# Optimization experiments

Measured on AMD Instinct MI355X. Metric: run time of the kernel, lower is better.

The kernel has to match this reference:

```python
import jax, jax.numpy as jnp
import numpy as np

B, N, D, H = 2, 2048, 1024, 16
HD = D // H
SCALE = HD ** -0.5


def setup_inputs() -> dict:
    key = jax.random.key(0)
    ks = jax.random.split(key, 5)
    s = D ** -0.5  # keep activations well-scaled like torch Linear init
    return {
        "x": jax.random.normal(ks[0], (B, N, D), jnp.float32),
        "Wq": jax.random.normal(ks[1], (D, D), jnp.float32) * s,
        "bq": jnp.zeros((D,), jnp.float32),
        "Wk": jax.random.normal(ks[2], (D, D), jnp.float32) * s,
        "bk": jnp.zeros((D,), jnp.float32),
        "Wv": jax.random.normal(ks[3], (D, D), jnp.float32) * s,
        "bv": jnp.zeros((D,), jnp.float32),
        "Wo": jax.random.normal(ks[4], (D, D), jnp.float32) * s,
        "bo": jnp.zeros((D,), jnp.float32),
    }


def reference(x, Wq, bq, Wk, bk, Wv, bv, Wo, bo):
    # projections: [B,N,D] -> [B,H,N,HD]
    def split_heads(t):
        return t.reshape(B, N, H, HD).transpose(0, 2, 1, 3)

    q = split_heads(x @ Wq + bq)
    k = split_heads(x @ Wk + bk)
    v = split_heads(x @ Wv + bv)
    # eager attention: explicit [B,H,N,N] scores, matching the torch module
    attn = jnp.einsum("bhnd,bhmd->bhnm", q, k) * SCALE
    attn = jax.nn.softmax(attn, axis=-1)
    out = jnp.einsum("bhnm,bhmd->bhnd", attn, v)
    out = out.transpose(0, 2, 1, 3).reshape(B, N, D)
    return out @ Wo + bo
```

## Files before the change

kernel.cpp:

```cpp
#include <hip/hip_runtime.h>
#include <hip/hip_bf16.h>

typedef __attribute__((ext_vector_type(8))) short bf16x8;
typedef __attribute__((ext_vector_type(4))) float f32x4;
typedef __attribute__((ext_vector_type(4))) unsigned short us4;
typedef __attribute__((ext_vector_type(8))) unsigned short us8;
typedef unsigned short u16;

#define NB 2
#define NSEQ 2048
#define DM 1024
#define NH 16
#define HD 64
#define NTOK (NB*NSEQ)
#define QK_SCALE (0.125f * 1.4426950408889634f)

__device__ __forceinline__ u16 f2b(float f) {
  __hip_bfloat16 h = __float2bfloat16(f);
  return __builtin_bit_cast(u16, h);
}

__device__ __forceinline__ unsigned cvtpk(float a, float b) {
  unsigned r;
  asm("v_cvt_pk_bf16_f32 %0, %1, %2" : "=v"(r) : "v"(a), "v"(b));
  return r;
}

__device__ __forceinline__ void gload16(const void* g, void* l) {
  __builtin_amdgcn_global_load_lds((__attribute__((address_space(1))) void*)g,
                                   (__attribute__((address_space(3))) void*)l, 16, 0, 0);
}

__global__ __launch_bounds__(256) void k_convx(const float* __restrict__ x, u16* __restrict__ xb) {
  const int idx = (blockIdx.x * 256 + threadIdx.x) * 8;
  const float4 v0 = *(const float4*)(x + idx);
  const float4 v1 = *(const float4*)(x + idx + 4);
  us8 o;
  o[0]=f2b(v0.x); o[1]=f2b(v0.y); o[2]=f2b(v0.z); o[3]=f2b(v0.w);
  o[4]=f2b(v1.x); o[5]=f2b(v1.y); o[6]=f2b(v1.z); o[7]=f2b(v1.w);
  *(us8*)(xb + idx) = o;
}

__global__ __launch_bounds__(256) void k_twt4(const float* __restrict__ W0, const float* __restrict__ W1,
                                              const float* __restrict__ W2, const float* __restrict__ W3,
                                              u16* __restrict__ T0, u16* __restrict__ T1,
                                              u16* __restrict__ T2, u16* __restrict__ T3) {
  const float* W = (blockIdx.z == 0) ? W0 : (blockIdx.z == 1) ? W1 : (blockIdx.z == 2) ? W2 : W3;
  u16* WT = (blockIdx.z == 0) ? T0 : (blockIdx.z == 1) ? T1 : (blockIdx.z == 2) ? T2 : T3;
  __shared__ float tile[64][68];
  const int n0 = blockIdx.x * 64, k0 = blockIdx.y * 64;
  const int tr = threadIdx.x >> 4, tc = (threadIdx.x & 15) * 4;
#pragma unroll
  for (int rr = 0; rr < 4; ++rr) {
    const int r = rr * 16 + tr;
    *(float4*)&tile[r][tc] = *(const float4*)&W[(size_t)(k0 + r) * DM + n0 + tc];
  }
  __syncthreads();
#pragma unroll
  for (int rr = 0; rr < 4; ++rr) {
    const int nr = rr * 16 + tr;
    us4 o;
#pragma unroll
    for (int e = 0; e < 4; ++e) o[e] = f2b(tile[tc + e][nr]);
    *(us4*)&WT[(size_t)(n0 + nr) * DM + k0 + tc] = o;
  }
}

__global__ __launch_bounds__(256) void k_gemm_qkv(
    const u16* __restrict__ xb,
    const u16* __restrict__ WqT, const u16* __restrict__ WkT, const u16* __restrict__ WvT,
    const float* __restrict__ bq, const float* __restrict__ bk, const float* __restrict__ bv,
    u16* __restrict__ Qb, u16* __restrict__ Kb, u16* __restrict__ Vtb)
{
  const int z = blockIdx.z;
  const bool isV = (z == 2);
  const u16* Ap = (z == 0) ? WqT : (z == 1) ? WkT : xb;
  const u16* Bt = isV ? WvT : xb;
  const float* bp = (z == 0) ? bq : (z == 1) ? bk : bv;
  const float scale = (z == 0) ? QK_SCALE : 1.0f;
  u16* outp = (z == 0) ? Qb : (z == 1) ? Kb : Vtb;
  const int i0 = isV ? blockIdx.x * 128 : blockIdx.y * 128;
  const int j0 = isV ? blockIdx.y * 128 : blockIdx.x * 128;

  __shared__ char smem[32 * 1024];
  const int tid = threadIdx.x, lane = tid & 63, wv = tid >> 6;
  const int li = lane & 15, g = lane >> 4;
  const int wi = wv >> 1, wj = wv & 1;

  f32x4 acc[4][4];
#pragma unroll
  for (int a = 0; a < 4; ++a)
#pragma unroll
    for (int b = 0; b < 4; ++b) acc[a][b] = f32x4{0.f, 0.f, 0.f, 0.f};

  auto stage = [&](int kt, int buf) {
#pragma unroll
    for (int c = 0; c < 2; ++c) {
      const int lg = c * 256 + tid;
      const int r = lg >> 2, ch = (lg & 3) ^ (r & 3);
      gload16(Ap + (size_t)(i0 + r) * 1024 + kt * 32 + ch * 8,
              smem + buf * 16384 + lg * 16);
      gload16(Bt + (size_t)(j0 + r) * 1024 + kt * 32 + ch * 8,
              smem + buf * 16384 + 8192 + lg * 16);
    }
  };

  stage(0, 0);

  for (int kt = 0; kt < 32; ++kt) {
    __syncthreads();
    if (kt + 1 < 32) stage(kt + 1, (kt + 1) & 1);
    const char* As = smem + (kt & 1) * 16384;
    const char* Bs = As + 8192;
    bf16x8 af[4], bfr[4];
#pragma unroll
    for (int it = 0; it < 4; ++it) {
      const int ri = 64 * wi + 16 * it + li;
      af[it] = *(const bf16x8*)(As + ri * 64 + ((g * 16) ^ ((ri & 3) << 4)));
      const int rj = 64 * wj + 16 * it + li;
      bfr[it] = *(const bf16x8*)(Bs + rj * 64 + ((g * 16) ^ ((rj & 3) << 4)));
    }
#pragma unroll
    for (int it = 0; it < 4; ++it)
#pragma unroll
      for (int jt = 0; jt < 4; ++jt)
        acc[it][jt] = __builtin_amdgcn_mfma_f32_16x16x32_bf16(af[it], bfr[jt], acc[it][jt], 0, 0, 0);
  }

#pragma unroll
  for (int it = 0; it < 4; ++it) {
    const int ib = i0 + 64 * wi + 16 * it + 4 * g;
    f32x4 b4;
    if (!isV) b4 = *(const f32x4*)(bp + ib);
#pragma unroll
    for (int jt = 0; jt < 4; ++jt) {
      const int j = j0 + 64 * wj + 16 * jt + li;
      f32x4 v = acc[it][jt];
      if (!isV) {
        v += b4;
        v *= scale;
        us4 pk; pk[0]=f2b(v[0]); pk[1]=f2b(v[1]); pk[2]=f2b(v[2]); pk[3]=f2b(v[3]);
        *(us4*)(outp + (size_t)j * 1024 + ib) = pk;
      } else {
        const float bj = bp[j];
        v[0] += bj; v[1] += bj; v[2] += bj; v[3] += bj;
        us4 pk; pk[0]=f2b(v[0]); pk[1]=f2b(v[1]); pk[2]=f2b(v[2]); pk[3]=f2b(v[3]);
        const size_t addr = ((size_t)(ib >> 11) * 1024 + j) * 2048 + (ib & 2047);
        *(us4*)(outp + addr) = pk;
      }
    }
  }
}

__global__ __launch_bounds__(256) void k_gemm_out(
    const u16* __restrict__ A, const u16* __restrict__ Bt, const float* __restrict__ bias,
    float* __restrict__ outp)
{
  __shared__ char smem[48 * 1024];
  const int tid = threadIdx.x, lane = tid & 63, wv = tid >> 6;
  const int li = lane & 15, g = lane >> 4;
  const int i0 = blockIdx.y * 128, j0 = blockIdx.x * 64;

  f32x4 acc[2][4];
#pragma unroll
  for (int a = 0; a < 2; ++a)
#pragma unroll
    for (int b = 0; b < 4; ++b) acc[a][b] = f32x4{0.f, 0.f, 0.f, 0.f};

  auto stage = [&](int kt, int buf) {
#pragma unroll
    for (int c = 0; c < 4; ++c) {
      const int lg = c * 256 + tid;
      const int r = lg >> 3, ch = (lg & 7) ^ (r & 7);
      gload16(A + (size_t)(i0 + r) * 1024 + kt * 64 + ch * 8,
              smem + buf * 24576 + lg * 16);
    }
#pragma unroll
    for (int c = 0; c < 2; ++c) {
      const int lg = c * 256 + tid;
      const int r = lg >> 3, ch = (lg & 7) ^ (r & 7);
      gload16(Bt + (size_t)(j0 + r) * 1024 + kt * 64 + ch * 8,
              smem + buf * 24576 + 16384 + lg * 16);
    }
  };

  stage(0, 0);

  for (int kt = 0; kt < 16; ++kt) {
    __syncthreads();
    if (kt + 1 < 16) stage(kt + 1, (kt + 1) & 1);
    const char* As = smem + (kt & 1) * 24576;
    const char* Bs = As + 16384;
#pragma unroll
    for (int ks = 0; ks < 2; ++ks) {
      bf16x8 af[2], bfr[4];
#pragma unroll
      for (int it = 0; it < 2; ++it) {
        const int ri = 32 * wv + 16 * it + li;
        af[it] = *(const bf16x8*)(As + ri * 128 + ((ks * 64 + g * 16) ^ ((ri & 7) << 4)));
      }
#pragma unroll
      for (int jt = 0; jt < 4; ++jt) {
        const int rj = 16 * jt + li;
        bfr[jt] = *(const bf16x8*)(Bs + rj * 128 + ((ks * 64 + g * 16) ^ ((rj & 7) << 4)));
      }
#pragma unroll
      for (int it = 0; it < 2; ++it)
#pragma unroll
        for (int jt = 0; jt < 4; ++jt)
          acc[it][jt] = __builtin_amdgcn_mfma_f32_16x16x32_bf16(af[it], bfr[jt], acc[it][jt], 0, 0, 0);
    }
  }

#pragma unroll
  for (int it = 0; it < 2; ++it) {
    const int ib = i0 + 32 * wv + 16 * it + 4 * g;
    const f32x4 b4 = *(const f32x4*)(bias + ib);
#pragma unroll
    for (int jt = 0; jt < 4; ++jt) {
      const int j = j0 + 16 * jt + li;
      f32x4 v = acc[it][jt] + b4;
      *(f32x4*)(outp + (size_t)j * 1024 + ib) = v;
    }
  }
}

__global__ __launch_bounds__(256, 2) void k_attn(const u16* __restrict__ Q, const u16* __restrict__ K,
                                                 const u16* __restrict__ Vt, u16* __restrict__ O)
{
  __shared__ char smem[48 * 1024];
  const int tid = threadIdx.x, lane = tid & 63, w = tid >> 6;
  const int li = lane & 15, g = lane >> 4;

  const int vid = blockIdx.x;
  const int u = vid >> 3;
  const int bh = (vid & 7) * 4 + (u >> 4);
  const int qt = u & 15;
  const int b = bh >> 4, h = bh & 15;
  const int n0 = qt * 128;
  const size_t tokbase = (size_t)b * NSEQ;
  const int iq = 16 * w + li;

  bf16x8 qf[2][2];
#pragma unroll
  for (int grp = 0; grp < 2; ++grp)
#pragma unroll
    for (int ks = 0; ks < 2; ++ks)
      qf[grp][ks] = *(const bf16x8*)(Q + (tokbase + n0 + 64 * grp + iq) * 1024 + h * 64 + 32 * ks + 8 * g);

  bf16x8 ones;
#pragma unroll
  for (int e = 0; e < 8; ++e) ones[e] = (short)0x3F80;

  f32x4 oacc[2][4];
#pragma unroll
  for (int grp = 0; grp < 2; ++grp)
#pragma unroll
    for (int dt = 0; dt < 4; ++dt) oacc[grp][dt] = f32x4{0.f, 0.f, 0.f, 0.f};
  f32x4 ls[2] = {f32x4{0.f,0.f,0.f,0.f}, f32x4{0.f,0.f,0.f,0.f}};

  const u16* Kb = K + tokbase * 1024 + h * 64;
  const u16* Vb = Vt + (size_t)bh * 64 * 2048;

  auto stage = [&](int t, int buf) {
    const int jn = t * 64;
#pragma unroll
    for (int c = 0; c < 2; ++c) {
      const int lg = c * 256 + tid;
      const int r = lg >> 3, ch = (lg & 7) ^ (r & 7);
      gload16(Kb + (size_t)(jn + r) * 1024 + ch * 8, smem + buf * 8192 + (c * 256 + w * 64) * 16);
      gload16(Vb + (size_t)r * 2048 + jn + ch * 8, smem + 16384 + buf * 8192 + (c * 256 + w * 64) * 16);
    }
  };

  auto tilebody = [&](int t, int buf) {
    __syncthreads();
    if (t + 1 < 32) stage(t + 1, buf ^ 1);
    const char* Ks = smem + buf * 8192;
    const char* Vs = smem + 16384 + buf * 8192;

    f32x4 s[2][4];
#pragma unroll
    for (int grp = 0; grp < 2; ++grp)
#pragma unroll
      for (int jt = 0; jt < 4; ++jt) s[grp][jt] = f32x4{0.f, 0.f, 0.f, 0.f};
#pragma unroll
    for (int ks = 0; ks < 2; ++ks) {
#pragma unroll
      for (int jt = 0; jt < 4; ++jt) {
        const int rj = 16 * jt + li;
        bf16x8 a = *(const bf16x8*)(Ks + rj * 128 + ((ks * 64 + g * 16) ^ ((rj & 7) << 4)));
        s[0][jt] = __builtin_amdgcn_mfma_f32_16x16x32_bf16(a, qf[0][ks], s[0][jt], 0, 0, 0);
        s[1][jt] = __builtin_amdgcn_mfma_f32_16x16x32_bf16(a, qf[1][ks], s[1][jt], 0, 0, 0);
      }
    }

#pragma unroll
    for (int grp = 0; grp < 2; ++grp) {
      const int row = iq + 64 * grp;
      char* Pr = smem + 32768 + row * 128;
      const int swz = (row & 7) << 4;
#pragma unroll
      for (int jt = 0; jt < 4; ++jt) {
        uint2 pk;
        pk.x = cvtpk(exp2f(s[grp][jt][0]), exp2f(s[grp][jt][1]));
        pk.y = cvtpk(exp2f(s[grp][jt][2]), exp2f(s[grp][jt][3]));
        *(uint2*)(Pr + ((32 * jt + 8 * g) ^ swz)) = pk;
      }
    }

#pragma unroll
    for (int ks = 0; ks < 2; ++ks) {
      const int kb = ks * 64 + g * 16;
      bf16x8 bpv0 = *(const bf16x8*)(smem + 32768 + iq * 128 + (kb ^ ((iq & 7) << 4)));
      bf16x8 bpv1 = *(const bf16x8*)(smem + 32768 + (iq + 64) * 128 + (kb ^ ((iq & 7) << 4)));
      ls[0] = __builtin_amdgcn_mfma_f32_16x16x32_bf16(ones, bpv0, ls[0], 0, 0, 0);
      ls[1] = __builtin_amdgcn_mfma_f32_16x16x32_bf16(ones, bpv1, ls[1], 0, 0, 0);
#pragma unroll
      for (int dt = 0; dt < 4; ++dt) {
        const int rd = 16 * dt + li;
        bf16x8 av = *(const bf16x8*)(Vs + rd * 128 + (kb ^ ((rd & 7) << 4)));
        oacc[0][dt] = __builtin_amdgcn_mfma_f32_16x16x32_bf16(av, bpv0, oacc[0][dt], 0, 0, 0);
        oacc[1][dt] = __builtin_amdgcn_mfma_f32_16x16x32_bf16(av, bpv1, oacc[1][dt], 0, 0, 0);
      }
    }
  };

  stage(0, 0);
#pragma unroll 1
  for (int tt = 0; tt < 16; ++tt) {
    tilebody(2 * tt, 0);
    tilebody(2 * tt + 1, 1);
  }

#pragma unroll
  for (int grp = 0; grp < 2; ++grp) {
    const float inv = 1.f / ls[grp][0];
    const size_t obase = (tokbase + n0 + 64 * grp + iq) * 1024 + h * 64;
#pragma unroll
    for (int dt = 0; dt < 4; ++dt) {
      us4 pk;
#pragma unroll
      for (int e = 0; e < 4; ++e) pk[e] = f2b(oacc[grp][dt][e] * inv);
      *(us4*)(O + obase + 16 * dt + 4 * g) = pk;
    }
  }
}

extern "C" void kernel_launch(void* const* d_in, const int* in_sizes, int n_in,
                              void* d_out, int out_size, void* d_ws, size_t ws_size,
                              hipStream_t stream) {
  const float* x  = (const float*)d_in[0];
  const float* Wq = (const float*)d_in[1];
  const float* bq = (const float*)d_in[2];
  const float* Wk = (const float*)d_in[3];
  const float* bk = (const float*)d_in[4];
  const float* Wv = (const float*)d_in[5];
  const float* bv = (const float*)d_in[6];
  const float* Wo = (const float*)d_in[7];
  const float* bo = (const float*)d_in[8];

  char* ws = (char*)d_ws;
  u16* xb  = (u16*)(ws);
  u16* WqT = (u16*)(ws + (8  << 20));
  u16* WkT = (u16*)(ws + (10 << 20));
  u16* WvT = (u16*)(ws + (12 << 20));
  u16* WoT = (u16*)(ws + (14 << 20));
  u16* Qb  = (u16*)(ws + (16 << 20));
  u16* Kb  = (u16*)(ws + (24 << 20));
  u16* Vtb = (u16*)(ws + (32 << 20));
  u16* Ob  = (u16*)(ws + (40 << 20));

  k_convx<<<2048, 256, 0, stream>>>(x, xb);
  k_twt4<<<dim3(16, 16, 4), 256, 0, stream>>>(Wq, Wk, Wv, Wo, WqT, WkT, WvT, WoT);

  k_gemm_qkv<<<dim3(32, 8, 3), 256, 0, stream>>>(xb, WqT, WkT, WvT, bq, bk, bv, Qb, Kb, Vtb);

  k_attn<<<512, 256, 0, stream>>>(Qb, Kb, Vtb, Ob);

  k_gemm_out<<<dim3(64, 8), 256, 0, stream>>>(WoT, Ob, bo, (float*)d_out);
}
```

Measured before the change: 123.0 us.

## Triple-buffer K/V tiles in attention and merge prep kernels into one launch

The attention kernel moves from double to triple buffering of K/V tiles. Loads are issued two tiles ahead, and explicit vmcnt waits plus raw barriers replace __syncthreads, so global loads overlap more compute. Shared memory per block grows from 48 to 64 KB, which may limit occupancy at two blocks per CU. Separately, the x conversion and weight transpose kernels are fused into a single launch to save one kernel launch.

Result: faster. 118.0 us (-4.0%).

```diff
diff --git a/kernel.cpp b/kernel.cpp
--- a/kernel.cpp
+++ b/kernel.cpp
@@ -31,24 +31,27 @@
                                    (__attribute__((address_space(3))) void*)l, 16, 0, 0);
 }
 
-__global__ __launch_bounds__(256) void k_convx(const float* __restrict__ x, u16* __restrict__ xb) {
-  const int idx = (blockIdx.x * 256 + threadIdx.x) * 8;
-  const float4 v0 = *(const float4*)(x + idx);
-  const float4 v1 = *(const float4*)(x + idx + 4);
-  us8 o;
-  o[0]=f2b(v0.x); o[1]=f2b(v0.y); o[2]=f2b(v0.z); o[3]=f2b(v0.w);
-  o[4]=f2b(v1.x); o[5]=f2b(v1.y); o[6]=f2b(v1.z); o[7]=f2b(v1.w);
-  *(us8*)(xb + idx) = o;
-}
-
-__global__ __launch_bounds__(256) void k_twt4(const float* __restrict__ W0, const float* __restrict__ W1,
+__global__ __launch_bounds__(256) void k_prep(const float* __restrict__ x, u16* __restrict__ xb,
+                                              const float* __restrict__ W0, const float* __restrict__ W1,
                                               const float* __restrict__ W2, const float* __restrict__ W3,
                                               u16* __restrict__ T0, u16* __restrict__ T1,
                                               u16* __restrict__ T2, u16* __restrict__ T3) {
-  const float* W = (blockIdx.z == 0) ? W0 : (blockIdx.z == 1) ? W1 : (blockIdx.z == 2) ? W2 : W3;
-  u16* WT = (blockIdx.z == 0) ? T0 : (blockIdx.z == 1) ? T1 : (blockIdx.z == 2) ? T2 : T3;
   __shared__ float tile[64][68];
-  const int n0 = blockIdx.x * 64, k0 = blockIdx.y * 64;
+  const int bid = blockIdx.x;
+  if (bid >= 1024) {
+    const int idx = ((bid - 1024) * 256 + threadIdx.x) * 8;
+    const float4 v0 = *(const float4*)(x + idx);
+    const float4 v1 = *(const float4*)(x + idx + 4);
+    us8 o;
+    o[0]=f2b(v0.x); o[1]=f2b(v0.y); o[2]=f2b(v0.z); o[3]=f2b(v0.w);
+    o[4]=f2b(v1.x); o[5]=f2b(v1.y); o[6]=f2b(v1.z); o[7]=f2b(v1.w);
+    *(us8*)(xb + idx) = o;
+    return;
+  }
+  const int bz = bid >> 8, by = (bid >> 4) & 15, bx = bid & 15;
+  const float* W = (bz == 0) ? W0 : (bz == 1) ? W1 : (bz == 2) ? W2 : W3;
+  u16* WT = (bz == 0) ? T0 : (bz == 1) ? T1 : (bz == 2) ? T2 : T3;
+  const int n0 = bx * 64, k0 = by * 64;
   const int tr = threadIdx.x >> 4, tc = (threadIdx.x & 15) * 4;
 #pragma unroll
   for (int rr = 0; rr < 4; ++rr) {
@@ -228,7 +231,7 @@
 __global__ __launch_bounds__(256, 2) void k_attn(const u16* __restrict__ Q, const u16* __restrict__ K,
                                                  const u16* __restrict__ Vt, u16* __restrict__ O)
 {
-  __shared__ char smem[48 * 1024];
+  __shared__ char smem[64 * 1024];
   const int tid = threadIdx.x, lane = tid & 63, w = tid >> 6;
   const int li = lane & 15, g = lane >> 4;
 
@@ -269,15 +272,13 @@
       const int lg = c * 256 + tid;
       const int r = lg >> 3, ch = (lg & 7) ^ (r & 7);
       gload16(Kb + (size_t)(jn + r) * 1024 + ch * 8, smem + buf * 8192 + (c * 256 + w * 64) * 16);
-      gload16(Vb + (size_t)r * 2048 + jn + ch * 8, smem + 16384 + buf * 8192 + (c * 256 + w * 64) * 16);
+      gload16(Vb + (size_t)r * 2048 + jn + ch * 8, smem + 24576 + buf * 8192 + (c * 256 + w * 64) * 16);
     }
   };
 
-  auto tilebody = [&](int t, int buf) {
-    __syncthreads();
-    if (t + 1 < 32) stage(t + 1, buf ^ 1);
+  auto body = [&](int t, int buf) {
     const char* Ks = smem + buf * 8192;
-    const char* Vs = smem + 16384 + buf * 8192;
+    const char* Vs = smem + 24576 + buf * 8192;
 
     f32x4 s[2][4];
 #pragma unroll
@@ -298,7 +299,7 @@
 #pragma unroll
     for (int grp = 0; grp < 2; ++grp) {
       const int row = iq + 64 * grp;
-      char* Pr = smem + 32768 + row * 128;
+      char* Pr = smem + 49152 + row * 128;
       const int swz = (row & 7) << 4;
 #pragma unroll
       for (int jt = 0; jt < 4; ++jt) {
@@ -312,8 +313,8 @@
 #pragma unroll
     for (int ks = 0; ks < 2; ++ks) {
       const int kb = ks * 64 + g * 16;
-      bf16x8 bpv0 = *(const bf16x8*)(smem + 32768 + iq * 128 + (kb ^ ((iq & 7) << 4)));
-      bf16x8 bpv1 = *(const bf16x8*)(smem + 32768 + (iq + 64) * 128 + (kb ^ ((iq & 7) << 4)));
+      bf16x8 bpv0 = *(const bf16x8*)(smem + 49152 + iq * 128 + (kb ^ ((iq & 7) << 4)));
+      bf16x8 bpv1 = *(const bf16x8*)(smem + 49152 + (iq + 64) * 128 + (kb ^ ((iq & 7) << 4)));
       ls[0] = __builtin_amdgcn_mfma_f32_16x16x32_bf16(ones, bpv0, ls[0], 0, 0, 0);
       ls[1] = __builtin_amdgcn_mfma_f32_16x16x32_bf16(ones, bpv1, ls[1], 0, 0, 0);
 #pragma unroll
@@ -327,11 +328,25 @@
   };
 
   stage(0, 0);
+  stage(1, 1);
+
 #pragma unroll 1
-  for (int tt = 0; tt < 16; ++tt) {
-    tilebody(2 * tt, 0);
-    tilebody(2 * tt + 1, 1);
-  }
+  for (int tt = 0; tt < 10; ++tt) {
+#pragma unroll
+    for (int uu = 0; uu < 3; ++uu) {
+      const int t = tt * 3 + uu;
+      asm volatile("s_waitcnt vmcnt(4)" ::: "memory");
+      __builtin_amdgcn_s_barrier();
+      stage(t + 2, (uu + 2) % 3);
+      body(t, uu);
+    }
+  }
+  asm volatile("s_waitcnt vmcnt(4)" ::: "memory");
+  __builtin_amdgcn_s_barrier();
+  body(30, 0);
+  asm volatile("s_waitcnt vmcnt(0)" ::: "memory");
+  __builtin_amdgcn_s_barrier();
+  body(31, 1);
 
 #pragma unroll
   for (int grp = 0; grp < 2; ++grp) {
@@ -371,8 +386,7 @@
   u16* Vtb = (u16*)(ws + (32 << 20));
   u16* Ob  = (u16*)(ws + (40 << 20));
 
-  k_convx<<<2048, 256, 0, stream>>>(x, xb);
-  k_twt4<<<dim3(16, 16, 4), 256, 0, stream>>>(Wq, Wk, Wv, Wo, WqT, WkT, WvT, WoT);
+  k_prep<<<3072, 256, 0, stream>>>(x, xb, Wq, Wk, Wv, Wo, WqT, WkT, WvT, WoT);
 
   k_gemm_qkv<<<dim3(32, 8, 3), 256, 0, stream>>>(xb, WqT, WkT, WvT, bq, bk, bv, Qb, Kb, Vtb);
 
```
